# Kernel tuning notes

Hardware: AMD Instinct MI355X
Metric: run time of the kernel (lower is better)

The kernel has to match this reference:

```python
import jax, jax.numpy as jnp
import numpy as np

B, C_IN, C_OUT, T, K, STRIDE, PAD = 16, 256, 256, 4096, 3, 1, 1


def deform_conv1d(x, offset, weight, bias):
    # x: (B,C,T); offset: (B,2K,Tout,1) interleaved (dy,dx); weight: (O,C,K); bias: (O,)
    Bn, C, Tn = x.shape
    O, _, Kn = weight.shape
    dy = offset[:, 0::2, :, 0]  # (B,K,Tout)
    dx = offset[:, 1::2, :, 0]  # (B,K,Tout)
    Tout = dy.shape[-1]
    # offset_mode='center': subtract dcn_base_offset (y base = k-pad, x base = 0)
    base_y = jnp.arange(Kn, dtype=x.dtype) - PAD
    dy = dy - base_y[None, :, None]
    # sampling position along T: t*stride - pad + k + dy
    t0 = jnp.arange(Tout, dtype=x.dtype) * STRIDE - PAD
    py = t0[None, None, :] + jnp.arange(Kn, dtype=x.dtype)[None, :, None] + dy  # (B,K,Tout)
    i0 = jnp.floor(py)
    frac = py - i0
    i0i = i0.astype(jnp.int32)

    def gather(idx):
        valid = ((idx >= 0) & (idx < Tn)).astype(x.dtype)  # zero padding outside
        idxc = jnp.clip(idx, 0, Tn - 1).reshape(Bn, 1, Kn * Tout)
        v = jnp.take_along_axis(x, jnp.broadcast_to(idxc, (Bn, C, Kn * Tout)), axis=2)
        return v.reshape(Bn, C, Kn, Tout) * valid[:, None]

    # linear interp along T
    v = gather(i0i) * (1.0 - frac)[:, None] + gather(i0i + 1) * frac[:, None]  # (B,C,K,Tout)
    # bilinear weight along the dummy width dim (W=1, base x index 0)
    wx = jnp.maximum(0.0, 1.0 - jnp.abs(dx))  # (B,K,Tout)
    v = v * wx[:, None]
    out = jnp.einsum('bckt,ock->bot', v, weight) + bias[None, :, None]
    return out


def setup_inputs() -> dict:
    key = jax.random.key(0)
    k1, k2, k3, k4 = jax.random.split(key, 4)
    x = jax.random.normal(k1, (B, C_IN, T), dtype=jnp.float32)
    offset = jax.random.normal(k2, (B, 2 * K, T, 1), dtype=jnp.float32)
    fan_in = C_IN * K
    bound = 1.0 / np.sqrt(fan_in)
    weight = jax.random.uniform(k3, (C_OUT, C_IN, K), minval=-bound, maxval=bound, dtype=jnp.float32)
    bias = jax.random.uniform(k4, (C_OUT,), minval=-bound, maxval=bound, dtype=jnp.float32)
    return {"x": x, "offset": offset, "weight": weight, "bias": bias}


def reference(x, offset, weight, bias):
    return deform_conv1d(x, offset, weight, bias)
```

## Files before the change

kernel.cpp:

```cpp
#include <hip/hip_runtime.h>
#include <hip/hip_bf16.h>

typedef __attribute__((ext_vector_type(8))) short bf16x8;
typedef __attribute__((ext_vector_type(4))) float f32x4;

constexpr int NB = 16, CIN = 256, COUT = 256, TDIM = 4096, KS = 3, PADV = 1;
constexpr int TT = 64;
constexpr int NSTEP = 12;

typedef __attribute__((address_space(1))) const unsigned int gu32;
typedef __attribute__((address_space(3))) unsigned int lu32;

static __device__ __forceinline__ ushort f2bf(float f) {
    union { __hip_bfloat16 h; ushort u; } cv;
    cv.h = __float2bfloat16(f);
    return cv.u;
}
static __device__ __forceinline__ float bf2f(ushort u) {
    union { unsigned int u32; float f; } cv;
    cv.u32 = ((unsigned int)u) << 16;
    return cv.f;
}

__global__ __launch_bounds__(256) void prepack_w2(const float* __restrict__ w,
                                                  __hip_bfloat16* __restrict__ wp2) {
    int idx = blockIdx.x * 256 + threadIdx.x;
    if (idx >= NSTEP * COUT * 64) return;
    int e    = idx & 7;
    int lane = (idx >> 3) & 63;
    int mf   = (idx >> 9) & 1;
    int kb   = (idx >> 10) & 1;
    int wid  = (idx >> 11) & 3;
    int ot   = (idx >> 13) & 1;
    int s    = idx >> 14;
    int o = ot * 128 + wid * 32 + mf * 16 + (lane & 15);
    int k = s % 3;
    int c = (s / 3) * 64 + kb * 32 + (lane >> 4) * 8 + e;
    wp2[idx] = __float2bfloat16(w[(o * CIN + c) * KS + k]);
}

__global__ __launch_bounds__(256) void prepack_w(const float* __restrict__ w,
                                                 __hip_bfloat16* __restrict__ wp) {
    int idx = blockIdx.x * 256 + threadIdx.x;
    if (idx >= NSTEP * COUT * 64) return;
    int e  = idx & 7;
    int j  = (idx >> 3) & 7;
    int o  = (idx >> 6) & (COUT - 1);
    int s  = idx >> 14;
    int k  = s % 3;
    int c  = (s / 3) * 64 + ((j ^ (o & 7)) << 3) + e;
    wp[idx] = __float2bfloat16(w[(o * CIN + c) * KS + k]);
}

__global__ __launch_bounds__(256) void transpose_x(const float* __restrict__ x,
                                                   ushort* __restrict__ xT) {
    __shared__ ushort tile[64][72];
    const int b  = blockIdx.z;
    const int c0 = blockIdx.y * 64;
    const int t0 = blockIdx.x * 64;
    const int tid = threadIdx.x;
    {
        const int c  = tid >> 2;
        const int tq = (tid & 3) << 4;
        const float* src = x + ((size_t)(b * CIN + c0 + c)) * TDIM + t0 + tq;
        #pragma unroll
        for (int i = 0; i < 4; ++i) {
            float4 f = *(const float4*)(src + 4 * i);
            tile[tq + 4 * i + 0][c] = f2bf(f.x);
            tile[tq + 4 * i + 1][c] = f2bf(f.y);
            tile[tq + 4 * i + 2][c] = f2bf(f.z);
            tile[tq + 4 * i + 3][c] = f2bf(f.w);
        }
    }
    __syncthreads();
    {
        const int t = tid >> 2;
        const int q = tid & 3;
        const uint4* lp = (const uint4*)&tile[t][q * 16];
        uint4 v0 = lp[0], v1 = lp[1];
        uint4* dst = (uint4*)(xT + ((size_t)b * TDIM + t0 + t) * CIN + c0 + q * 16);
        dst[0] = v0;
        dst[1] = v1;
    }
}

__global__ __launch_bounds__(256, 4) void deform_mfma_xt(
    const ushort* __restrict__ xT,
    const float* __restrict__ off,
    const ushort* __restrict__ wp2,
    const float* __restrict__ bias,
    float* __restrict__ out)
{
    __shared__ ushort v_s[TT * 64];
    __shared__ int4   sP[KS][TT];

    const int tid = threadIdx.x;

    const int bid = blockIdx.x;
    const int q   = bid & 7;
    const int r   = bid >> 3;
    const int b   = 2 * q + (r >> 7);
    const int r2  = r & 127;
    const int ot  = r2 >> 6;
    const int tt0 = (r2 & 63) * TT;

    if (tid < KS * TT) {
        int k = tid >> 6, j = tid & (TT - 1);
        int t = tt0 + j;
        float dyr = off[((b * 2 * KS + 2 * k) * TDIM) + t];
        float dxr = off[((b * 2 * KS + 2 * k + 1) * TDIM) + t];
        float dyk = dyr - (float)(k - PADV);
        float py  = (float)(t - PADV + k) + dyk;
        float i0f = floorf(py);
        float fr  = py - i0f;
        int i0 = (int)i0f, i1 = i0 + 1;
        float wx = fmaxf(0.0f, 1.0f - fabsf(dxr));
        float w0 = (1.0f - fr) * wx * ((i0 >= 0 && i0 < TDIM) ? 1.0f : 0.0f);
        float w1 = fr * wx * ((i1 >= 0 && i1 < TDIM) ? 1.0f : 0.0f);
        int base = min(max(i0, 0), TDIM - 2);
        bool iA = (i0 == base);
        float wa = iA ? w0 : ((i0 + 1 == base) ? w1 : 0.0f);
        float wb = iA ? w1 : ((i0 == base + 1) ? w0 : 0.0f);
        int4 p;
        p.x = base;
        p.y = __float_as_int(wa);
        p.z = __float_as_int(wb);
        p.w = 0;
        sP[k][j] = p;
    }

    const int wid  = tid >> 6;
    const int lane = tid & 63;
    const int lr   = lane & 15;
    const int lg   = lane >> 4;

    const int tg   = tid >> 3;
    const int slot = tid & 7;
    const int t0l  = tg;
    const int t1l  = tg + 32;
    const int voffA = (t0l * 128 + slot * 16) ^ ((t0l & 7) << 4);
    const int voffB = (t1l * 128 + slot * 16) ^ ((t1l & 7) << 4);

    f32x4 acc[2][4];
    #pragma unroll
    for (int i = 0; i < 2; ++i)
        #pragma unroll
        for (int j = 0; j < 4; ++j) acc[i][j] = (f32x4)0.0f;

    const ushort* xTb = xT + (size_t)b * TDIM * CIN;

    __syncthreads();

    bf16x8 af0, af1, af2, af3;
    bf16x8 pk0, pk1;
    {
        const ushort* wslot = wp2 + (size_t)(((0 * 2 + ot) * 4 + wid) * 4) * 512 + lane * 8;
        af0 = *(const bf16x8*)(wslot);
        af1 = *(const bf16x8*)(wslot + 512);
        af2 = *(const bf16x8*)(wslot + 1024);
        af3 = *(const bf16x8*)(wslot + 1536);
        int4 e0 = sP[0][t0l];
        int4 e1 = sP[0][t1l];
        const ushort* rowA = xTb + (size_t)e0.x * CIN + slot * 8;
        const ushort* rowB = xTb + (size_t)e1.x * CIN + slot * 8;
        bf16x8 a0 = *(const bf16x8*)rowA;
        bf16x8 a1 = *(const bf16x8*)(rowA + CIN);
        bf16x8 b0 = *(const bf16x8*)rowB;
        bf16x8 b1 = *(const bf16x8*)(rowB + CIN);
        float wa0 = __int_as_float(e0.y), wb0 = __int_as_float(e0.z);
        float wa1 = __int_as_float(e1.y), wb1 = __int_as_float(e1.z);
        #pragma unroll
        for (int i = 0; i < 8; ++i) {
            pk0[i] = (short)f2bf(bf2f((ushort)a0[i]) * wa0 + bf2f((ushort)a1[i]) * wb0);
            pk1[i] = (short)f2bf(bf2f((ushort)b0[i]) * wa1 + bf2f((ushort)b1[i]) * wb1);
        }
    }

    #pragma unroll 1
    for (int s = 0; s < NSTEP; ++s) {
        const int sn  = (s + 1 < NSTEP) ? s + 1 : NSTEP - 1;
        const int kn  = sn % 3;
        const int cbn = (sn / 3) * 64;

        __builtin_amdgcn_s_barrier();
        __builtin_amdgcn_sched_barrier(0);

        *(bf16x8*)((char*)v_s + voffA) = pk0;
        *(bf16x8*)((char*)v_s + voffB) = pk1;

        const ushort* wslot = wp2 + (size_t)(((sn * 2 + ot) * 4 + wid) * 4) * 512 + lane * 8;
        bf16x8 an0 = *(const bf16x8*)(wslot);
        bf16x8 an1 = *(const bf16x8*)(wslot + 512);
        bf16x8 an2 = *(const bf16x8*)(wslot + 1024);
        bf16x8 an3 = *(const bf16x8*)(wslot + 1536);

        int4 e0 = sP[kn][t0l];
        int4 e1 = sP[kn][t1l];
        const ushort* rowA = xTb + (size_t)e0.x * CIN + cbn + slot * 8;
        const ushort* rowB = xTb + (size_t)e1.x * CIN + cbn + slot * 8;
        bf16x8 ga0 = *(const bf16x8*)rowA;
        bf16x8 ga1 = *(const bf16x8*)(rowA + CIN);
        bf16x8 gb0 = *(const bf16x8*)rowB;
        bf16x8 gb1 = *(const bf16x8*)(rowB + CIN);

        __builtin_amdgcn_sched_barrier(0);
        asm volatile("s_waitcnt lgkmcnt(0)" ::: "memory");
        __builtin_amdgcn_sched_barrier(0);
        __builtin_amdgcn_s_barrier();
        __builtin_amdgcn_sched_barrier(0);

        #pragma unroll
        for (int kb = 0; kb < 2; ++kb) {
            const int kk = kb * 32 + lg * 8;
            bf16x8 bfr[4];
            #pragma unroll
            for (int nf = 0; nf < 4; ++nf) {
                int tc = nf * 16 + lr;
                int byte = (tc * 128 + kk * 2) ^ ((tc & 7) << 4);
                bfr[nf] = *(const bf16x8*)((const char*)v_s + byte);
            }
            bf16x8 a0 = kb ? af2 : af0;
            bf16x8 a1 = kb ? af3 : af1;
            #pragma unroll
            for (int nf = 0; nf < 4; ++nf) {
                acc[0][nf] = __builtin_amdgcn_mfma_f32_16x16x32_bf16(a0, bfr[nf], acc[0][nf], 0, 0, 0);
                acc[1][nf] = __builtin_amdgcn_mfma_f32_16x16x32_bf16(a1, bfr[nf], acc[1][nf], 0, 0, 0);
            }
        }
        __builtin_amdgcn_sched_barrier(0);

        {
            float wa0 = __int_as_float(e0.y), wb0 = __int_as_float(e0.z);
            float wa1 = __int_as_float(e1.y), wb1 = __int_as_float(e1.z);
            #pragma unroll
            for (int i = 0; i < 8; ++i) {
                pk0[i] = (short)f2bf(bf2f((ushort)ga0[i]) * wa0 + bf2f((ushort)ga1[i]) * wb0);
                pk1[i] = (short)f2bf(bf2f((ushort)gb0[i]) * wa1 + bf2f((ushort)gb1[i]) * wb1);
            }
        }
        af0 = an0; af1 = an1; af2 = an2; af3 = an3;
    }

    #pragma unroll
    for (int mf = 0; mf < 2; ++mf) {
        #pragma unroll
        for (int rg = 0; rg < 4; ++rg) {
            int o = ot * 128 + wid * 32 + mf * 16 + lg * 4 + rg;
            float bv = bias[o];
            float* orow = out + (size_t)(b * COUT + o) * TDIM + tt0;
            #pragma unroll
            for (int nf = 0; nf < 4; ++nf)
                orow[nf * 16 + lr] = acc[mf][nf][rg] + bv;
        }
    }
}

__global__ __launch_bounds__(512, 4) void deform_mfma_gather(
    const float* __restrict__ x,
    const float* __restrict__ off,
    const __hip_bfloat16* __restrict__ wp,
    const float* __restrict__ bias,
    float* __restrict__ out)
{
    __shared__ ushort w_s[COUT * 64];
    __shared__ ushort v_s[128 * 64];
    __shared__ int4   sP[KS][128];

    const int tid = threadIdx.x;
    const int bid  = blockIdx.x;
    const int q    = bid & 7;
    const int r    = bid >> 3;
    const int b    = 2 * q + (r >> 5);
    const int tt0  = (r & 31) * 128;

    if (tid < KS * 128) {
        int k = tid >> 7, j = tid & 127;
        int t = tt0 + j;
        float dyr = off[((b * 2 * KS + 2 * k) * TDIM) + t];
        float dxr = off[((b * 2 * KS + 2 * k + 1) * TDIM) + t];
        float py  = (float)(t - PADV + k) + dyr - (float)(k - PADV);
        float i0f = floorf(py);
        float fr  = py - i0f;
        int i0 = (int)i0f, i1 = i0 + 1;
        float wx = fmaxf(0.0f, 1.0f - fabsf(dxr));
        float w0 = (1.0f - fr) * wx * ((i0 >= 0 && i0 < TDIM) ? 1.0f : 0.0f);
        float w1 = fr * wx * ((i1 >= 0 && i1 < TDIM) ? 1.0f : 0.0f);
        int4 p;
        p.x = min(max(i0, 0), TDIM - 1);
        p.y = min(max(i1, 0), TDIM - 1);
        p.z = __float_as_int(w0);
        p.w = __float_as_int(w1);
        sP[k][j] = p;
    }

    const int wid    = tid >> 6;
    const int lane   = tid & 63;
    const int o_base = (wid >> 1) * 64;
    const int t_base = (wid & 1) * 64;
    const int lr     = lane & 15;
    const int lg     = lane >> 4;

    f32x4 acc[4][4];
    #pragma unroll
    for (int i = 0; i < 4; ++i)
        #pragma unroll
        for (int j = 0; j < 4; ++j) acc[i][j] = (f32x4)0.0f;

    const float* xb = x + (size_t)b * CIN * TDIM;

    for (int cb = 0; cb < 4; ++cb) {
      for (int k = 0; k < 3; ++k) {
        const int s_idx = cb * 3 + k;
        const int c0    = cb * 64;
        __syncthreads();
        {
            const char* gbase = (const char*)wp + (size_t)s_idx * 32768 + wid * 4096 + lane * 16;
            char* lbase = (char*)w_s + wid * 4096;
            #pragma unroll
            for (int i = 0; i < 4; ++i)
                __builtin_amdgcn_global_load_lds((gu32*)(gbase + i * 1024),
                                                 (lu32*)(lbase + i * 1024), 16, 0, 0);
        }
        {
            const int coct0 = tid >> 7;
            const int t     = tid & 127;
            int4 p = sP[k][t];
            const float* xr0 = xb + (size_t)(c0 + coct0 * 8) * TDIM;
            const float* xr1 = xr0 + (size_t)32 * TDIM;
            float g0[16], g1[16];
            #pragma unroll
            for (int i = 0; i < 8; ++i) {
                g0[2 * i]     = xr0[p.x];
                g0[2 * i + 1] = xr0[p.y];
                xr0 += TDIM;
            }
            #pragma unroll
            for (int i = 0; i < 8; ++i) {
                g1[2 * i]     = xr1[p.x];
                g1[2 * i + 1] = xr1[p.y];
                xr1 += TDIM;
            }
            float w0 = __int_as_float(p.z), w1 = __int_as_float(p.w);
            bf16x8 pk0, pk1;
            #pragma unroll
            for (int i = 0; i < 8; ++i) {
                pk0[i] = (short)f2bf(g0[2 * i] * w0 + g0[2 * i + 1] * w1);
                pk1[i] = (short)f2bf(g1[2 * i] * w0 + g1[2 * i + 1] * w1);
            }
            int row = t * 128;
            int swz = (t & 7) << 4;
            *(bf16x8*)((char*)v_s + ((row + coct0 * 16) ^ swz))       = pk0;
            *(bf16x8*)((char*)v_s + ((row + (coct0 + 4) * 16) ^ swz)) = pk1;
        }
        __syncthreads();
        #pragma unroll
        for (int kb = 0; kb < 2; ++kb) {
            const int kk = kb * 32 + lg * 8;
            bf16x8 bfr[4];
            #pragma unroll
            for (int nf = 0; nf < 4; ++nf) {
                int tc = t_base + nf * 16 + lr;
                int byte = (tc * 128 + kk * 2) ^ ((tc & 7) << 4);
                bfr[nf] = *(const bf16x8*)((const char*)v_s + byte);
            }
            #pragma unroll
            for (int mf = 0; mf < 4; ++mf) {
                int o  = o_base + mf * 16 + lr;
                int byte = (o * 128 + kk * 2) ^ ((o & 7) << 4);
                bf16x8 af = *(const bf16x8*)((const char*)w_s + byte);
                #pragma unroll
                for (int nf = 0; nf < 4; ++nf)
                    acc[mf][nf] = __builtin_amdgcn_mfma_f32_16x16x32_bf16(
                        af, bfr[nf], acc[mf][nf], 0, 0, 0);
            }
        }
      }
    }

    #pragma unroll
    for (int mf = 0; mf < 4; ++mf) {
        #pragma unroll
        for (int rg = 0; rg < 4; ++rg) {
            int o = o_base + mf * 16 + lg * 4 + rg;
            float bv = bias[o];
            float* orow = out + (size_t)(b * COUT + o) * TDIM + tt0 + t_base;
            #pragma unroll
            for (int nf = 0; nf < 4; ++nf)
                orow[nf * 16 + lr] = acc[mf][nf][rg] + bv;
        }
    }
}

extern "C" void kernel_launch(void* const* d_in, const int* in_sizes, int n_in,
                              void* d_out, int out_size, void* d_ws, size_t ws_size,
                              hipStream_t stream) {
    const float* x    = (const float*)d_in[0];
    const float* off  = (const float*)d_in[1];
    const float* w    = (const float*)d_in[2];
    const float* bias = (const float*)d_in[3];
    float* out = (float*)d_out;

    const size_t xt_off  = 512 * 1024;
    const size_t xt_need = xt_off + (size_t)NB * TDIM * CIN * sizeof(ushort);

    if (ws_size >= xt_need) {
        ushort* wp2 = (ushort*)d_ws;
        ushort* xT  = (ushort*)((char*)d_ws + xt_off);
        prepack_w2<<<dim3(768), dim3(256), 0, stream>>>(w, (__hip_bfloat16*)wp2);
        transpose_x<<<dim3(TDIM / 64, CIN / 64, NB), dim3(256), 0, stream>>>(x, xT);
        deform_mfma_xt<<<dim3(2048), dim3(256), 0, stream>>>(xT, off, wp2, bias, out);
    } else {
        __hip_bfloat16* wp = (__hip_bfloat16*)d_ws;
        prepack_w<<<dim3(768), dim3(256), 0, stream>>>(w, wp);
        deform_mfma_gather<<<dim3(512), dim3(512), 0, stream>>>(x, off, wp, bias, out);
    }
}
```

Baseline: 70.86 us.

## Widen reduction step to 128 channels, halving barrier-separated loop iterations

Each main-loop step now covers 128 input channels instead of 64, so the loop runs 6 steps instead of 12. Each thread gathers and interpolates 16 channels per row into a two-half LDS buffer. The weight prepack layout is changed to match. Weight fragments are now loaded at the top of the current step instead of being prefetched one step ahead. This halves the number of barriers and per-step overheads, but raises register pressure and exposes weight-load latency inside each step.

```diff
diff --git a/kernel.cpp b/kernel.cpp
--- a/kernel.cpp
+++ b/kernel.cpp
@@ -6,7 +6,8 @@
 
 constexpr int NB = 16, CIN = 256, COUT = 256, TDIM = 4096, KS = 3, PADV = 1;
 constexpr int TT = 64;
-constexpr int NSTEP = 12;
+constexpr int NSTEP = 6;
+constexpr int NSTEP_FB = 12;
 
 typedef __attribute__((address_space(1))) const unsigned int gu32;
 typedef __attribute__((address_space(3))) unsigned int lu32;
@@ -25,24 +26,24 @@
 __global__ __launch_bounds__(256) void prepack_w2(const float* __restrict__ w,
                                                   __hip_bfloat16* __restrict__ wp2) {
     int idx = blockIdx.x * 256 + threadIdx.x;
-    if (idx >= NSTEP * COUT * 64) return;
+    if (idx >= NSTEP * 32768) return;
     int e    = idx & 7;
     int lane = (idx >> 3) & 63;
     int mf   = (idx >> 9) & 1;
-    int kb   = (idx >> 10) & 1;
-    int wid  = (idx >> 11) & 3;
-    int ot   = (idx >> 13) & 1;
-    int s    = idx >> 14;
+    int kb   = (idx >> 10) & 3;
+    int wid  = (idx >> 12) & 3;
+    int ot   = (idx >> 14) & 1;
+    int s    = idx >> 15;
     int o = ot * 128 + wid * 32 + mf * 16 + (lane & 15);
     int k = s % 3;
-    int c = (s / 3) * 64 + kb * 32 + (lane >> 4) * 8 + e;
+    int c = (s / 3) * 128 + kb * 32 + (lane >> 4) * 8 + e;
     wp2[idx] = __float2bfloat16(w[(o * CIN + c) * KS + k]);
 }
 
 __global__ __launch_bounds__(256) void prepack_w(const float* __restrict__ w,
                                                  __hip_bfloat16* __restrict__ wp) {
     int idx = blockIdx.x * 256 + threadIdx.x;
-    if (idx >= NSTEP * COUT * 64) return;
+    if (idx >= NSTEP_FB * COUT * 64) return;
     int e  = idx & 7;
     int j  = (idx >> 3) & 7;
     int o  = (idx >> 6) & (COUT - 1);
@@ -91,7 +92,7 @@
     const float* __restrict__ bias,
     float* __restrict__ out)
 {
-    __shared__ ushort v_s[TT * 64];
+    __shared__ ushort v_s[2][TT * 64];
     __shared__ int4   sP[KS][TT];
 
     const int tid = threadIdx.x;
@@ -136,10 +137,17 @@
 
     const int tg   = tid >> 3;
     const int slot = tid & 7;
+    const int half = slot >> 2;
+    const int cloc = (slot & 3) * 16;
     const int t0l  = tg;
     const int t1l  = tg + 32;
-    const int voffA = (t0l * 128 + slot * 16) ^ ((t0l & 7) << 4);
-    const int voffB = (t1l * 128 + slot * 16) ^ ((t1l & 7) << 4);
+    const int swA  = (t0l & 7) << 4;
+    const int swB  = (t1l & 7) << 4;
+    const int wA0  = (t0l * 128 + cloc * 2)      ^ swA;
+    const int wA1  = (t0l * 128 + cloc * 2 + 16) ^ swA;
+    const int wB0  = (t1l * 128 + cloc * 2)      ^ swB;
+    const int wB1  = (t1l * 128 + cloc * 2 + 16) ^ swB;
+    char* vhalf = (char*)v_s[half];
 
     f32x4 acc[2][4];
     #pragma unroll
@@ -151,28 +159,28 @@
 
     __syncthreads();
 
-    bf16x8 af0, af1, af2, af3;
-    bf16x8 pk0, pk1;
+    bf16x8 pkA0, pkA1, pkB0, pkB1;
     {
-        const ushort* wslot = wp2 + (size_t)(((0 * 2 + ot) * 4 + wid) * 4) * 512 + lane * 8;
-        af0 = *(const bf16x8*)(wslot);
-        af1 = *(const bf16x8*)(wslot + 512);
-        af2 = *(const bf16x8*)(wslot + 1024);
-        af3 = *(const bf16x8*)(wslot + 1536);
         int4 e0 = sP[0][t0l];
         int4 e1 = sP[0][t1l];
-        const ushort* rowA = xTb + (size_t)e0.x * CIN + slot * 8;
-        const ushort* rowB = xTb + (size_t)e1.x * CIN + slot * 8;
-        bf16x8 a0 = *(const bf16x8*)rowA;
-        bf16x8 a1 = *(const bf16x8*)(rowA + CIN);
-        bf16x8 b0 = *(const bf16x8*)rowB;
-        bf16x8 b1 = *(const bf16x8*)(rowB + CIN);
+        const ushort* rowA = xTb + (size_t)e0.x * CIN + slot * 16;
+        const ushort* rowB = xTb + (size_t)e1.x * CIN + slot * 16;
+        bf16x8 a0a = *(const bf16x8*)rowA;
+        bf16x8 a0b = *(const bf16x8*)(rowA + 8);
+        bf16x8 a1a = *(const bf16x8*)(rowA + CIN);
+        bf16x8 a1b = *(const bf16x8*)(rowA + CIN + 8);
+        bf16x8 b0a = *(const bf16x8*)rowB;
+        bf16x8 b0b = *(const bf16x8*)(rowB + 8);
+        bf16x8 b1a = *(const bf16x8*)(rowB + CIN);
+        bf16x8 b1b = *(const bf16x8*)(rowB + CIN + 8);
         float wa0 = __int_as_float(e0.y), wb0 = __int_as_float(e0.z);
         float wa1 = __int_as_float(e1.y), wb1 = __int_as_float(e1.z);
         #pragma unroll
         for (int i = 0; i < 8; ++i) {
-            pk0[i] = (short)f2bf(bf2f((ushort)a0[i]) * wa0 + bf2f((ushort)a1[i]) * wb0);
-            pk1[i] = (short)f2bf(bf2f((ushort)b0[i]) * wa1 + bf2f((ushort)b1[i]) * wb1);
+            pkA0[i] = (short)f2bf(bf2f((ushort)a0a[i]) * wa0 + bf2f((ushort)a1a[i]) * wb0);
+            pkA1[i] = (short)f2bf(bf2f((ushort)a0b[i]) * wa0 + bf2f((ushort)a1b[i]) * wb0);
+            pkB0[i] = (short)f2bf(bf2f((ushort)b0a[i]) * wa1 + bf2f((ushort)b1a[i]) * wb1);
+            pkB1[i] = (short)f2bf(bf2f((ushort)b0b[i]) * wa1 + bf2f((ushort)b1b[i]) * wb1);
         }
     }
 
@@ -180,28 +188,36 @@
     for (int s = 0; s < NSTEP; ++s) {
         const int sn  = (s + 1 < NSTEP) ? s + 1 : NSTEP - 1;
         const int kn  = sn % 3;
-        const int cbn = (sn / 3) * 64;
+        const int cbn = (sn / 3) * 128;
 
         __builtin_amdgcn_s_barrier();
         __builtin_amdgcn_sched_barrier(0);
 
-        *(bf16x8*)((char*)v_s + voffA) = pk0;
-        *(bf16x8*)((char*)v_s + voffB) = pk1;
-
-        const ushort* wslot = wp2 + (size_t)(((sn * 2 + ot) * 4 + wid) * 4) * 512 + lane * 8;
-        bf16x8 an0 = *(const bf16x8*)(wslot);
-        bf16x8 an1 = *(const bf16x8*)(wslot + 512);
-        bf16x8 an2 = *(const bf16x8*)(wslot + 1024);
-        bf16x8 an3 = *(const bf16x8*)(wslot + 1536);
+        *(bf16x8*)(vhalf + wA0) = pkA0;
+        *(bf16x8*)(vhalf + wA1) = pkA1;
+        *(bf16x8*)(vhalf + wB0) = pkB0;
+        *(bf16x8*)(vhalf + wB1) = pkB1;
+
+        const ushort* wbase = wp2 + (size_t)((s * 2 + ot) * 4 + wid) * 4096 + lane * 8;
+        bf16x8 af[4][2];
+        #pragma unroll
+        for (int kb = 0; kb < 4; ++kb) {
+            af[kb][0] = *(const bf16x8*)(wbase + kb * 1024);
+            af[kb][1] = *(const bf16x8*)(wbase + kb * 1024 + 512);
+        }
 
         int4 e0 = sP[kn][t0l];
         int4 e1 = sP[kn][t1l];
-        const ushort* rowA = xTb + (size_t)e0.x * CIN + cbn + slot * 8;
-        const ushort* rowB = xTb + (size_t)e1.x * CIN + cbn + slot * 8;
-        bf16x8 ga0 = *(const bf16x8*)rowA;
-        bf16x8 ga1 = *(const bf16x8*)(rowA + CIN);
-        bf16x8 gb0 = *(const bf16x8*)rowB;
-        bf16x8 gb1 = *(const bf16x8*)(rowB + CIN);
+        const ushort* rowA = xTb + (size_t)e0.x * CIN + cbn + slot * 16;
+        const ushort* rowB = xTb + (size_t)e1.x * CIN + cbn + slot * 16;
+        bf16x8 ga0a = *(const bf16x8*)rowA;
+        bf16x8 ga0b = *(const bf16x8*)(rowA + 8);
+        bf16x8 ga1a = *(const bf16x8*)(rowA + CIN);
+        bf16x8 ga1b = *(const bf16x8*)(rowA + CIN + 8);
+        bf16x8 gb0a = *(const bf16x8*)rowB;
+        bf16x8 gb0b = *(const bf16x8*)(rowB + 8);
+        bf16x8 gb1a = *(const bf16x8*)(rowB + CIN);
+        bf16x8 gb1b = *(const bf16x8*)(rowB + CIN + 8);
 
         __builtin_amdgcn_sched_barrier(0);
         asm volatile("s_waitcnt lgkmcnt(0)" ::: "memory");
@@ -210,21 +226,20 @@
         __builtin_amdgcn_sched_barrier(0);
 
         #pragma unroll
-        for (int kb = 0; kb < 2; ++kb) {
-            const int kk = kb * 32 + lg * 8;
+        for (int kb = 0; kb < 4; ++kb) {
+            const int hh  = kb >> 1;
+            const int kk2 = (kb & 1) * 32 + lg * 8;
             bf16x8 bfr[4];
             #pragma unroll
             for (int nf = 0; nf < 4; ++nf) {
                 int tc = nf * 16 + lr;
-                int byte = (tc * 128 + kk * 2) ^ ((tc & 7) << 4);
-                bfr[nf] = *(const bf16x8*)((const char*)v_s + byte);
-            }
-            bf16x8 a0 = kb ? af2 : af0;
-            bf16x8 a1 = kb ? af3 : af1;
+                int byte = (tc * 128 + kk2 * 2) ^ ((tc & 7) << 4);
+                bfr[nf] = *(const bf16x8*)((const char*)v_s[hh] + byte);
+            }
             #pragma unroll
             for (int nf = 0; nf < 4; ++nf) {
-                acc[0][nf] = __builtin_amdgcn_mfma_f32_16x16x32_bf16(a0, bfr[nf], acc[0][nf], 0, 0, 0);
-                acc[1][nf] = __builtin_amdgcn_mfma_f32_16x16x32_bf16(a1, bfr[nf], acc[1][nf], 0, 0, 0);
+                acc[0][nf] = __builtin_amdgcn_mfma_f32_16x16x32_bf16(af[kb][0], bfr[nf], acc[0][nf], 0, 0, 0);
+                acc[1][nf] = __builtin_amdgcn_mfma_f32_16x16x32_bf16(af[kb][1], bfr[nf], acc[1][nf], 0, 0, 0);
             }
         }
         __builtin_amdgcn_sched_barrier(0);
@@ -234,11 +249,12 @@
             float wa1 = __int_as_float(e1.y), wb1 = __int_as_float(e1.z);
             #pragma unroll
             for (int i = 0; i < 8; ++i) {
-                pk0[i] = (short)f2bf(bf2f((ushort)ga0[i]) * wa0 + bf2f((ushort)ga1[i]) * wb0);
-                pk1[i] = (short)f2bf(bf2f((ushort)gb0[i]) * wa1 + bf2f((ushort)gb1[i]) * wb1);
-            }
-        }
-        af0 = an0; af1 = an1; af2 = an2; af3 = an3;
+                pkA0[i] = (short)f2bf(bf2f((ushort)ga0a[i]) * wa0 + bf2f((ushort)ga1a[i]) * wb0);
+                pkA1[i] = (short)f2bf(bf2f((ushort)ga0b[i]) * wa0 + bf2f((ushort)ga1b[i]) * wb0);
+                pkB0[i] = (short)f2bf(bf2f((ushort)gb0a[i]) * wa1 + bf2f((ushort)gb1a[i]) * wb1);
+                pkB1[i] = (short)f2bf(bf2f((ushort)gb0b[i]) * wa1 + bf2f((ushort)gb1b[i]) * wb1);
+            }
+        }
     }
 
     #pragma unroll
```

Measured after the change: 71.22 us. Within noise of the previous version (+0.5%).
